# Optimization experiments

Measured on AMD Instinct MI355X. Metric: run time of the kernel, lower is better.

Reference implementation:

```python
import jax, jax.numpy as jnp
import numpy as np

N_NODES = 50000
N_EDGES = 300000
D_IN = 256
D_HID = 256
N_LAYERS = 3
D_OUT = 32
NUM_GRAPHS = 512


def setup_inputs() -> dict:
    key = jax.random.key(0)
    ks = jax.random.split(key, 10)
    x = jax.random.normal(ks[0], (N_NODES, D_IN), dtype=jnp.float32)
    edge_index = jax.random.randint(ks[1], (2, N_EDGES), 0, N_NODES, dtype=jnp.int64)
    batch = jnp.sort(jax.random.randint(ks[2], (N_NODES,), 0, NUM_GRAPHS, dtype=jnp.int64))
    # GraphConv params: out_i = relu(lin_rel(sum_j x_j) + lin_root(x_i)), bias in lin_rel.
    # in_channels == hidden_channels so all nc layers stack into one tensor.
    s = 1.0 / np.sqrt(D_HID)
    W_rel = jax.random.normal(ks[3], (N_LAYERS, D_HID, D_HID), dtype=jnp.float32) * s
    W_root = jax.random.normal(ks[4], (N_LAYERS, D_HID, D_HID), dtype=jnp.float32) * s
    b_conv = jax.random.normal(ks[5], (N_LAYERS, D_HID), dtype=jnp.float32) * s
    W1 = jax.random.normal(ks[6], (D_HID, 4 * D_HID), dtype=jnp.float32) * s
    b1 = jnp.zeros((4 * D_HID,), dtype=jnp.float32)
    W2 = jax.random.normal(ks[7], (4 * D_HID, D_OUT), dtype=jnp.float32) * (1.0 / np.sqrt(4 * D_HID))
    b2 = jnp.zeros((D_OUT,), dtype=jnp.float32)
    return {"x": x, "edge_index": edge_index, "batch": batch,
            "W_rel": W_rel, "W_root": W_root, "b_conv": b_conv,
            "W1": W1, "b1": b1, "W2": W2, "b2": b2,
            "num_graphs": NUM_GRAPHS}


def reference(x, edge_index, batch, W_rel, W_root, b_conv, W1, b1, W2, b2, num_graphs):
    src, dst = edge_index[0], edge_index[1]
    n = x.shape[0]
    # stacked GraphConv(aggr='add') layers with ReLU
    for i in range(W_rel.shape[0]):
        aggr = jax.ops.segment_sum(x[src], dst, num_segments=n)  # [N, d] gather+scatter-add
        x = jax.nn.relu(aggr @ W_rel[i] + x @ W_root[i] + b_conv[i])
    # global_add_pool over graph ids
    pooled = jax.ops.segment_sum(x, batch, num_segments=num_graphs)  # [G, d]
    h = jax.nn.relu(pooled @ W1 + b1)
    return jax.nn.sigmoid(h @ W2 + b2)
```

## Files before the change

### kernel.cpp

```cpp
#include <hip/hip_runtime.h>
#include <math.h>

#define NNODES 50000
#define MPAD   50048
#define D      256
#define K2     512
#define NEDGES 300000
#define NGRAPH 512
#define NLAYERS 3

#define SCB    256
#define NSCB   ((NNODES + SCB - 1) / SCB)

typedef __bf16 bf16x8 __attribute__((ext_vector_type(8)));
typedef float  f32x4  __attribute__((ext_vector_type(4)));

__device__ __forceinline__ ushort f2bf(float f) {
    unsigned u = __float_as_uint(f);
    unsigned r = (u + 0x7FFFu + ((u >> 16) & 1u)) >> 16;
    return (ushort)r;
}
__device__ __forceinline__ float bf2f(ushort b) {
    return __uint_as_float(((unsigned)b) << 16);
}

__device__ __forceinline__ void stage16(const ushort* g, ushort* l) {
    __builtin_amdgcn_global_load_lds(
        (const __attribute__((address_space(1))) unsigned*)g,
        (__attribute__((address_space(3))) unsigned*)l, 16, 0, 0);
}

__global__ __launch_bounds__(256)
void hist_kernel(const int* __restrict__ dst, int* __restrict__ deg, int nE) {
    int e = blockIdx.x * 256 + threadIdx.x;
    if (e < nE) atomicAdd(&deg[dst[e]], 1);
}

__global__ __launch_bounds__(SCB)
void scan_part_kernel(const int* __restrict__ deg, int* __restrict__ bsum) {
    __shared__ int red[SCB];
    int t = threadIdx.x;
    int i = blockIdx.x * SCB + t;
    red[t] = (i < NNODES) ? deg[i] : 0;
    __syncthreads();
#pragma unroll
    for (int off = SCB / 2; off > 0; off >>= 1) {
        if (t < off) red[t] += red[t + off];
        __syncthreads();
    }
    if (t == 0) bsum[blockIdx.x] = red[0];
}

__global__ __launch_bounds__(256)
void scan_bsum_kernel(const int* __restrict__ bsum, int* __restrict__ boff) {
    __shared__ int p[256];
    int t = threadIdx.x;
    p[t] = (t < NSCB) ? bsum[t] : 0;
    __syncthreads();
    for (int off = 1; off < 256; off <<= 1) {
        int v = (t >= off) ? p[t - off] : 0;
        __syncthreads();
        p[t] += v;
        __syncthreads();
    }
    if (t < NSCB) boff[t] = (t == 0) ? 0 : p[t - 1];
}

__global__ __launch_bounds__(SCB)
void scan_final_kernel(const int* __restrict__ deg, const int* __restrict__ boff,
                       int* __restrict__ row_start, int* __restrict__ cursor) {
    __shared__ int p[SCB];
    int t = threadIdx.x;
    int i = blockIdx.x * SCB + t;
    int v = (i < NNODES) ? deg[i] : 0;
    p[t] = v;
    __syncthreads();
    for (int off = 1; off < SCB; off <<= 1) {
        int u = (t >= off) ? p[t - off] : 0;
        __syncthreads();
        p[t] += u;
        __syncthreads();
    }
    int excl = boff[blockIdx.x] + p[t] - v;
    if (i < NNODES) {
        row_start[i] = excl;
        cursor[i] = excl;
    }
    if (blockIdx.x == 0 && t == 0) row_start[NNODES] = NEDGES;
}

__global__ __launch_bounds__(256)
void fill_kernel(const int* __restrict__ src, const int* __restrict__ dst,
                 int* __restrict__ cursor, int* __restrict__ e_src, int nE) {
    int e = blockIdx.x * 256 + threadIdx.x;
    if (e < nE) {
        int pos = atomicAdd(&cursor[dst[e]], 1);
        e_src[pos] = src[e];
    }
}

__global__ __launch_bounds__(256)
void gstart_kernel(const int* __restrict__ batch, int* __restrict__ gstart) {
    int g = blockIdx.x * 256 + threadIdx.x;
    if (g > NGRAPH) return;
    if (g == NGRAPH) { gstart[g] = NNODES; return; }
    int lo = 0, hi = NNODES;
    while (lo < hi) { int mid = (lo + hi) >> 1; if (batch[mid] < g) lo = mid + 1; else hi = mid; }
    gstart[g] = lo;
}

__global__ __launch_bounds__(256)
void prep_w_kernel(const float* __restrict__ W_rel, const float* __restrict__ W_root,
                   ushort* __restrict__ Wh, ushort* __restrict__ Wl) {
    int i = blockIdx.x * 256 + threadIdx.x;
    if (i >= NLAYERS * D * K2) return;
    int L = i / (D * K2);
    int rem = i % (D * K2);
    int n = rem / K2;
    int k = rem % K2;
    float v = (k < D) ? W_rel[(size_t)L * D * D + (size_t)k * D + n]
                      : W_root[(size_t)L * D * D + (size_t)(k - D) * D + n];
    ushort hi = f2bf(v);
    float  lo = v - bf2f(hi);
    Wh[i] = hi;
    Wl[i] = f2bf(lo);
}

__global__ __launch_bounds__(256)
void gather_f32_kernel(const float* __restrict__ x,
                       const int* __restrict__ row_start,
                       const int* __restrict__ e_src,
                       float* __restrict__ aggr) {
    int t = threadIdx.x;
    int n = blockIdx.x * 4 + (t >> 6);
    if (n >= NNODES) return;
    int lane = t & 63;
    int beg = row_start[n], end = row_start[n + 1];
    float a0 = 0.f, a1 = 0.f, a2 = 0.f, a3 = 0.f;
    int j = beg;
    for (; j + 4 <= end; j += 4) {
        int s0 = e_src[j], s1 = e_src[j + 1], s2 = e_src[j + 2], s3 = e_src[j + 3];
        float4 v0 = *reinterpret_cast<const float4*>(x + (size_t)s0 * D + lane * 4);
        float4 v1 = *reinterpret_cast<const float4*>(x + (size_t)s1 * D + lane * 4);
        float4 v2 = *reinterpret_cast<const float4*>(x + (size_t)s2 * D + lane * 4);
        float4 v3 = *reinterpret_cast<const float4*>(x + (size_t)s3 * D + lane * 4);
        a0 += v0.x + v1.x + v2.x + v3.x;
        a1 += v0.y + v1.y + v2.y + v3.y;
        a2 += v0.z + v1.z + v2.z + v3.z;
        a3 += v0.w + v1.w + v2.w + v3.w;
    }
    for (; j < end; ++j) {
        int s = e_src[j];
        float4 v = *reinterpret_cast<const float4*>(x + (size_t)s * D + lane * 4);
        a0 += v.x; a1 += v.y; a2 += v.z; a3 += v.w;
    }
    float4 o; o.x = a0; o.y = a1; o.z = a2; o.w = a3;
    *reinterpret_cast<float4*>(aggr + (size_t)n * D + lane * 4) = o;
}

#define GBM 128
#define GBN 128
#define GBK 32

__global__ __launch_bounds__(256)
void gemm_split_kernel(const float* __restrict__ A,
                       const float* __restrict__ X,
                       const ushort* __restrict__ Wh,
                       const ushort* __restrict__ Wl,
                       const float* __restrict__ bias,
                       float* __restrict__ out) {
    __shared__ ushort Ah[GBM * GBK];
    __shared__ ushort Al[GBM * GBK];
    __shared__ ushort Bh[GBN * GBK];
    __shared__ ushort Bl[GBN * GBK];

    int t = threadIdx.x;
    int wid = t >> 6, lane = t & 63;
    int m0 = blockIdx.x * GBM;
    int n0 = blockIdx.y * GBN;
    int wr = wid >> 1, wc = wid & 1;

    f32x4 acc[4][4];
#pragma unroll
    for (int m = 0; m < 4; ++m)
#pragma unroll
        for (int n = 0; n < 4; ++n)
            acc[m][n] = (f32x4){0.f, 0.f, 0.f, 0.f};

    int arow = t >> 1;
    int acb  = (t & 1) * 2;
    int aswz = (arow >> 1) & 3;
    int gr   = m0 + arow;
    bool arow_ok = (gr < NNODES);

    for (int k0 = 0; k0 < K2; k0 += GBK) {
        const float* Asrc = (k0 < D) ? A : X;
        int kk = k0 & (D - 1);

#pragma unroll
        for (int op = 0; op < 2; ++op) {
            int idx = op * 256 + wid * 64 + lane;
            int row = idx >> 2, sub = idx & 3;
            int kh = ((row >> 1) & 3) ^ sub;
            stage16(Wh + (size_t)(n0 + row) * K2 + k0 + kh * 8, Bh + (size_t)(op * 256 + wid * 64) * 8);
            stage16(Wl + (size_t)(n0 + row) * K2 + k0 + kh * 8, Bl + (size_t)(op * 256 + wid * 64) * 8);
        }

        {
            const float* base = Asrc + (size_t)gr * D + kk + acb * 8;
            float4 v0, v1, v2, v3;
            if (arow_ok) {
                v0 = *reinterpret_cast<const float4*>(base + 0);
                v1 = *reinterpret_cast<const float4*>(base + 4);
                v2 = *reinterpret_cast<const float4*>(base + 8);
                v3 = *reinterpret_cast<const float4*>(base + 12);
            } else {
                v0 = v1 = v2 = v3 = make_float4(0.f, 0.f, 0.f, 0.f);
            }
            float vv[16] = {v0.x, v0.y, v0.z, v0.w, v1.x, v1.y, v1.z, v1.w,
                            v2.x, v2.y, v2.z, v2.w, v3.x, v3.y, v3.z, v3.w};
            ushort hi[16], lo[16];
#pragma unroll
            for (int i = 0; i < 16; ++i) {
                hi[i] = f2bf(vv[i]);
                lo[i] = f2bf(vv[i] - bf2f(hi[i]));
            }
            int p0 = aswz ^ acb;
            int p1 = aswz ^ (acb + 1);
            *reinterpret_cast<uint4*>(&Ah[arow * GBK + p0 * 8]) = *reinterpret_cast<const uint4*>(&hi[0]);
            *reinterpret_cast<uint4*>(&Ah[arow * GBK + p1 * 8]) = *reinterpret_cast<const uint4*>(&hi[8]);
            *reinterpret_cast<uint4*>(&Al[arow * GBK + p0 * 8]) = *reinterpret_cast<const uint4*>(&lo[0]);
            *reinterpret_cast<uint4*>(&Al[arow * GBK + p1 * 8]) = *reinterpret_cast<const uint4*>(&lo[8]);
        }
        __syncthreads();

        bf16x8 ah[4], al[4], bh[4], bl[4];
        int half = lane >> 4;
#pragma unroll
        for (int m = 0; m < 4; ++m) {
            int row = wr * 64 + m * 16 + (lane & 15);
            int off = row * GBK + ((((row >> 1) & 3) ^ half) * 8);
            ah[m] = *reinterpret_cast<const bf16x8*>(&Ah[off]);
            al[m] = *reinterpret_cast<const bf16x8*>(&Al[off]);
        }
#pragma unroll
        for (int n = 0; n < 4; ++n) {
            int row = wc * 64 + n * 16 + (lane & 15);
            int off = row * GBK + ((((row >> 1) & 3) ^ half) * 8);
            bh[n] = *reinterpret_cast<const bf16x8*>(&Bh[off]);
            bl[n] = *reinterpret_cast<const bf16x8*>(&Bl[off]);
        }
#pragma unroll
        for (int m = 0; m < 4; ++m)
#pragma unroll
            for (int n = 0; n < 4; ++n) {
                acc[m][n] = __builtin_amdgcn_mfma_f32_16x16x32_bf16(ah[m], bh[n], acc[m][n], 0, 0, 0);
                acc[m][n] = __builtin_amdgcn_mfma_f32_16x16x32_bf16(ah[m], bl[n], acc[m][n], 0, 0, 0);
                acc[m][n] = __builtin_amdgcn_mfma_f32_16x16x32_bf16(al[m], bh[n], acc[m][n], 0, 0, 0);
            }
        __syncthreads();
    }

    int half = lane >> 4;
#pragma unroll
    for (int n = 0; n < 4; ++n) {
        int col = n0 + wc * 64 + n * 16 + (lane & 15);
        float bv = bias[col];
#pragma unroll
        for (int m = 0; m < 4; ++m) {
            int rbase = m0 + wr * 64 + m * 16 + half * 4;
#pragma unroll
            for (int j = 0; j < 4; ++j) {
                int r = rbase + j;
                if (r < NNODES)
                    out[(size_t)r * D + col] = fmaxf(acc[m][n][j] + bv, 0.f);
            }
        }
    }
}

__global__ __launch_bounds__(256)
void pool_seg_kernel(const float* __restrict__ x, const int* __restrict__ gstart,
                     float* __restrict__ pooled) {
    __shared__ float red[4][D];
    int g = blockIdx.x;
    int t = threadIdx.x, wid = t >> 6, lane = t & 63;
    int beg = gstart[g], end = gstart[g + 1];
    float a0 = 0.f, a1 = 0.f, a2 = 0.f, a3 = 0.f;
    for (int r = beg + wid; r < end; r += 4) {
        float4 v = *reinterpret_cast<const float4*>(x + (size_t)r * D + lane * 4);
        a0 += v.x; a1 += v.y; a2 += v.z; a3 += v.w;
    }
    red[wid][lane * 4 + 0] = a0;
    red[wid][lane * 4 + 1] = a1;
    red[wid][lane * 4 + 2] = a2;
    red[wid][lane * 4 + 3] = a3;
    __syncthreads();
    float s = red[0][t] + red[1][t] + red[2][t] + red[3][t];
    pooled[(size_t)g * D + t] = s;
}

__global__ __launch_bounds__(256)
void mlp1_kernel(const float* __restrict__ pooled, const float* __restrict__ W1,
                 const float* __restrict__ b1, float* __restrict__ h) {
    __shared__ float p[D];
    int g = blockIdx.x, t = threadIdx.x;
    p[t] = pooled[(size_t)g * D + t];
    __syncthreads();
    float4 acc = make_float4(0.f, 0.f, 0.f, 0.f);
    for (int k = 0; k < D; ++k) {
        float4 w = *reinterpret_cast<const float4*>(W1 + (size_t)k * 1024 + t * 4);
        float pv = p[k];
        acc.x += pv * w.x; acc.y += pv * w.y; acc.z += pv * w.z; acc.w += pv * w.w;
    }
    float4 b = *reinterpret_cast<const float4*>(b1 + t * 4);
    acc.x = fmaxf(acc.x + b.x, 0.f);
    acc.y = fmaxf(acc.y + b.y, 0.f);
    acc.z = fmaxf(acc.z + b.z, 0.f);
    acc.w = fmaxf(acc.w + b.w, 0.f);
    *reinterpret_cast<float4*>(h + (size_t)g * 1024 + t * 4) = acc;
}

__global__ __launch_bounds__(256)
void mlp2_kernel(const float* __restrict__ h, const float* __restrict__ W2,
                 const float* __restrict__ b2, float* __restrict__ out) {
    __shared__ float red[8][32];
    int g = blockIdx.x, t = threadIdx.x;
    int c = t & 31, kc = t >> 5;
    float s = 0.f;
    const float* hr = h + (size_t)g * 1024;
    for (int k = kc * 128; k < kc * 128 + 128; ++k)
        s += hr[k] * W2[(size_t)k * 32 + c];
    red[kc][c] = s;
    __syncthreads();
    if (t < 32) {
        float v = b2[t];
#pragma unroll
        for (int i = 0; i < 8; ++i) v += red[i][t];
        out[(size_t)g * 32 + t] = 1.f / (1.f + expf(-v));
    }
}

extern "C" void kernel_launch(void* const* d_in, const int* in_sizes, int n_in,
                              void* d_out, int out_size, void* d_ws, size_t ws_size,
                              hipStream_t stream) {
    const float* x      = (const float*)d_in[0];
    const int*   ei     = (const int*)d_in[1];
    const int*   batch  = (const int*)d_in[2];
    const float* W_rel  = (const float*)d_in[3];
    const float* W_root = (const float*)d_in[4];
    const float* b_conv = (const float*)d_in[5];
    const float* W1     = (const float*)d_in[6];
    const float* b1     = (const float*)d_in[7];
    const float* W2     = (const float*)d_in[8];
    const float* b2     = (const float*)d_in[9];
    float* outp = (float*)d_out;

    const size_t NF = (size_t)MPAD * D;
    float* aggr   = (float*)d_ws;
    float* buf0   = aggr + NF;
    float* buf1   = buf0 + NF;
    ushort* Wh    = (ushort*)(buf1 + NF);
    ushort* Wl    = Wh + (size_t)NLAYERS * D * K2;
    float* pooled = (float*)(Wl + (size_t)NLAYERS * D * K2);
    float* hbuf   = pooled + (size_t)NGRAPH * D;
    int* deg       = (int*)(hbuf + (size_t)NGRAPH * 1024);
    int* row_start = deg + NNODES;
    int* cursor    = row_start + NNODES + 1;
    int* e_src     = cursor + NNODES;
    int* gstart    = e_src + NEDGES;
    int* bsum      = gstart + NGRAPH + 1;
    int* boff      = bsum + NSCB;

    const int* srcp = ei;
    const int* dstp = ei + NEDGES;

    hipMemsetAsync(deg, 0, NNODES * sizeof(int), stream);
    hist_kernel<<<(NEDGES + 255) / 256, 256, 0, stream>>>(dstp, deg, NEDGES);
    scan_part_kernel<<<NSCB, SCB, 0, stream>>>(deg, bsum);
    scan_bsum_kernel<<<1, 256, 0, stream>>>(bsum, boff);
    scan_final_kernel<<<NSCB, SCB, 0, stream>>>(deg, boff, row_start, cursor);
    fill_kernel<<<(NEDGES + 255) / 256, 256, 0, stream>>>(srcp, dstp, cursor, e_src, NEDGES);
    gstart_kernel<<<3, 256, 0, stream>>>(batch, gstart);

    prep_w_kernel<<<(NLAYERS * D * K2 + 255) / 256, 256, 0, stream>>>(W_rel, W_root, Wh, Wl);

    int gatherBlocks = (NNODES + 3) / 4;
    dim3 ggrid(MPAD / GBM, D / GBN);

    const float* cur = x;
    float* nxt = buf0;
    for (int L = 0; L < NLAYERS; ++L) {
        gather_f32_kernel<<<gatherBlocks, 256, 0, stream>>>(cur, row_start, e_src, aggr);
        gemm_split_kernel<<<ggrid, 256, 0, stream>>>(aggr, cur,
                                                     Wh + (size_t)L * D * K2,
                                                     Wl + (size_t)L * D * K2,
                                                     b_conv + (size_t)L * D,
                                                     nxt);
        cur = nxt;
        nxt = (nxt == buf0) ? buf1 : buf0;
    }

    pool_seg_kernel<<<NGRAPH, 256, 0, stream>>>(cur, gstart, pooled);
    mlp1_kernel<<<NGRAPH, 256, 0, stream>>>(pooled, W1, b1, hbuf);
    mlp2_kernel<<<NGRAPH, 256, 0, stream>>>(hbuf, W2, b2, outp);
}
```

Baseline: 459.8 us.

## Store activations as pre-split bf16 hi/lo pairs across gather, GEMM and pool

Activations and aggregates are now kept as two bf16 arrays (high and residual) instead of fp32. The GEMM stages its A operand with async 16-byte copies into LDS rather than loading fp32 and splitting per tile, and the gather and pool kernels read and write the split format. This moves the split work out of the GEMM inner loop and lets A staging use the same path as B. In exchange it adds a one-time conversion kernel for x and extra conversion work in the gather and GEMM epilogue, and the GEMM epilogue now does scalar 2-byte stores. Gather traffic per edge stays about the same because two 8-byte loads replace one 16-byte load.

```diff
diff --git a/kernel.cpp b/kernel.cpp
--- a/kernel.cpp
+++ b/kernel.cpp
@@ -127,10 +127,32 @@
 }
 
 __global__ __launch_bounds__(256)
-void gather_f32_kernel(const float* __restrict__ x,
-                       const int* __restrict__ row_start,
-                       const int* __restrict__ e_src,
-                       float* __restrict__ aggr) {
+void cvt_x_kernel(const float* __restrict__ x, ushort* __restrict__ xh,
+                  ushort* __restrict__ xl) {
+    size_t base = ((size_t)blockIdx.x * 256 + threadIdx.x) * 8;
+    if (base >= (size_t)MPAD * D) return;
+    ushort h[8], l[8];
+    if (base < (size_t)NNODES * D) {
+        float4 v0 = *reinterpret_cast<const float4*>(x + base);
+        float4 v1 = *reinterpret_cast<const float4*>(x + base + 4);
+        float vv[8] = {v0.x, v0.y, v0.z, v0.w, v1.x, v1.y, v1.z, v1.w};
+#pragma unroll
+        for (int j = 0; j < 8; ++j) {
+            h[j] = f2bf(vv[j]);
+            l[j] = f2bf(vv[j] - bf2f(h[j]));
+        }
+    } else {
+#pragma unroll
+        for (int j = 0; j < 8; ++j) { h[j] = 0; l[j] = 0; }
+    }
+    *reinterpret_cast<uint4*>(xh + base) = *reinterpret_cast<uint4*>(h);
+    *reinterpret_cast<uint4*>(xl + base) = *reinterpret_cast<uint4*>(l);
+}
+
+__global__ __launch_bounds__(256)
+void gather_hl_kernel(const ushort* __restrict__ ph, const ushort* __restrict__ pl,
+                      const int* __restrict__ row_start, const int* __restrict__ e_src,
+                      ushort* __restrict__ gh, ushort* __restrict__ gl) {
     int t = threadIdx.x;
     int n = blockIdx.x * 4 + (t >> 6);
     if (n >= NNODES) return;
@@ -140,22 +162,39 @@
     int j = beg;
     for (; j + 4 <= end; j += 4) {
         int s0 = e_src[j], s1 = e_src[j + 1], s2 = e_src[j + 2], s3 = e_src[j + 3];
-        float4 v0 = *reinterpret_cast<const float4*>(x + (size_t)s0 * D + lane * 4);
-        float4 v1 = *reinterpret_cast<const float4*>(x + (size_t)s1 * D + lane * 4);
-        float4 v2 = *reinterpret_cast<const float4*>(x + (size_t)s2 * D + lane * 4);
-        float4 v3 = *reinterpret_cast<const float4*>(x + (size_t)s3 * D + lane * 4);
-        a0 += v0.x + v1.x + v2.x + v3.x;
-        a1 += v0.y + v1.y + v2.y + v3.y;
-        a2 += v0.z + v1.z + v2.z + v3.z;
-        a3 += v0.w + v1.w + v2.w + v3.w;
+        ushort4 h0 = *reinterpret_cast<const ushort4*>(ph + (size_t)s0 * D + lane * 4);
+        ushort4 l0 = *reinterpret_cast<const ushort4*>(pl + (size_t)s0 * D + lane * 4);
+        ushort4 h1 = *reinterpret_cast<const ushort4*>(ph + (size_t)s1 * D + lane * 4);
+        ushort4 l1 = *reinterpret_cast<const ushort4*>(pl + (size_t)s1 * D + lane * 4);
+        ushort4 h2 = *reinterpret_cast<const ushort4*>(ph + (size_t)s2 * D + lane * 4);
+        ushort4 l2 = *reinterpret_cast<const ushort4*>(pl + (size_t)s2 * D + lane * 4);
+        ushort4 h3 = *reinterpret_cast<const ushort4*>(ph + (size_t)s3 * D + lane * 4);
+        ushort4 l3 = *reinterpret_cast<const ushort4*>(pl + (size_t)s3 * D + lane * 4);
+        a0 += (bf2f(h0.x) + bf2f(l0.x)) + (bf2f(h1.x) + bf2f(l1.x)) +
+              (bf2f(h2.x) + bf2f(l2.x)) + (bf2f(h3.x) + bf2f(l3.x));
+        a1 += (bf2f(h0.y) + bf2f(l0.y)) + (bf2f(h1.y) + bf2f(l1.y)) +
+              (bf2f(h2.y) + bf2f(l2.y)) + (bf2f(h3.y) + bf2f(l3.y));
+        a2 += (bf2f(h0.z) + bf2f(l0.z)) + (bf2f(h1.z) + bf2f(l1.z)) +
+              (bf2f(h2.z) + bf2f(l2.z)) + (bf2f(h3.z) + bf2f(l3.z));
+        a3 += (bf2f(h0.w) + bf2f(l0.w)) + (bf2f(h1.w) + bf2f(l1.w)) +
+              (bf2f(h2.w) + bf2f(l2.w)) + (bf2f(h3.w) + bf2f(l3.w));
     }
     for (; j < end; ++j) {
         int s = e_src[j];
-        float4 v = *reinterpret_cast<const float4*>(x + (size_t)s * D + lane * 4);
-        a0 += v.x; a1 += v.y; a2 += v.z; a3 += v.w;
-    }
-    float4 o; o.x = a0; o.y = a1; o.z = a2; o.w = a3;
-    *reinterpret_cast<float4*>(aggr + (size_t)n * D + lane * 4) = o;
+        ushort4 h = *reinterpret_cast<const ushort4*>(ph + (size_t)s * D + lane * 4);
+        ushort4 l = *reinterpret_cast<const ushort4*>(pl + (size_t)s * D + lane * 4);
+        a0 += bf2f(h.x) + bf2f(l.x);
+        a1 += bf2f(h.y) + bf2f(l.y);
+        a2 += bf2f(h.z) + bf2f(l.z);
+        a3 += bf2f(h.w) + bf2f(l.w);
+    }
+    ushort4 oh, ol;
+    oh.x = f2bf(a0); ol.x = f2bf(a0 - bf2f(oh.x));
+    oh.y = f2bf(a1); ol.y = f2bf(a1 - bf2f(oh.y));
+    oh.z = f2bf(a2); ol.z = f2bf(a2 - bf2f(oh.z));
+    oh.w = f2bf(a3); ol.w = f2bf(a3 - bf2f(oh.w));
+    *reinterpret_cast<ushort4*>(gh + (size_t)n * D + lane * 4) = oh;
+    *reinterpret_cast<ushort4*>(gl + (size_t)n * D + lane * 4) = ol;
 }
 
 #define GBM 128
@@ -163,16 +202,15 @@
 #define GBK 32
 
 __global__ __launch_bounds__(256)
-void gemm_split_kernel(const float* __restrict__ A,
-                       const float* __restrict__ X,
-                       const ushort* __restrict__ Wh,
-                       const ushort* __restrict__ Wl,
-                       const float* __restrict__ bias,
-                       float* __restrict__ out) {
-    __shared__ ushort Ah[GBM * GBK];
-    __shared__ ushort Al[GBM * GBK];
-    __shared__ ushort Bh[GBN * GBK];
-    __shared__ ushort Bl[GBN * GBK];
+void gemm_hl_kernel(const ushort* __restrict__ Gh, const ushort* __restrict__ Gl,
+                    const ushort* __restrict__ Xh, const ushort* __restrict__ Xl,
+                    const ushort* __restrict__ Wh, const ushort* __restrict__ Wl,
+                    const float* __restrict__ bias,
+                    ushort* __restrict__ outh, ushort* __restrict__ outl) {
+    __shared__ ushort AhS[GBM * GBK];
+    __shared__ ushort AlS[GBM * GBK];
+    __shared__ ushort BhS[GBN * GBK];
+    __shared__ ushort BlS[GBN * GBK];
 
     int t = threadIdx.x;
     int wid = t >> 6, lane = t & 63;
@@ -187,14 +225,9 @@
         for (int n = 0; n < 4; ++n)
             acc[m][n] = (f32x4){0.f, 0.f, 0.f, 0.f};
 
-    int arow = t >> 1;
-    int acb  = (t & 1) * 2;
-    int aswz = (arow >> 1) & 3;
-    int gr   = m0 + arow;
-    bool arow_ok = (gr < NNODES);
-
     for (int k0 = 0; k0 < K2; k0 += GBK) {
-        const float* Asrc = (k0 < D) ? A : X;
+        const ushort* ah = (k0 < D) ? Gh : Xh;
+        const ushort* al = (k0 < D) ? Gl : Xl;
         int kk = k0 & (D - 1);
 
 #pragma unroll
@@ -202,61 +235,37 @@
             int idx = op * 256 + wid * 64 + lane;
             int row = idx >> 2, sub = idx & 3;
             int kh = ((row >> 1) & 3) ^ sub;
-            stage16(Wh + (size_t)(n0 + row) * K2 + k0 + kh * 8, Bh + (size_t)(op * 256 + wid * 64) * 8);
-            stage16(Wl + (size_t)(n0 + row) * K2 + k0 + kh * 8, Bl + (size_t)(op * 256 + wid * 64) * 8);
+            size_t ldso = (size_t)(op * 256 + wid * 64) * 8;
+            stage16(ah + (size_t)(m0 + row) * D + kk + kh * 8, AhS + ldso);
+            stage16(al + (size_t)(m0 + row) * D + kk + kh * 8, AlS + ldso);
+            stage16(Wh + (size_t)(n0 + row) * K2 + k0 + kh * 8, BhS + ldso);
+            stage16(Wl + (size_t)(n0 + row) * K2 + k0 + kh * 8, BlS + ldso);
         }
-
-        {
-            const float* base = Asrc + (size_t)gr * D + kk + acb * 8;
-            float4 v0, v1, v2, v3;
-            if (arow_ok) {
-                v0 = *reinterpret_cast<const float4*>(base + 0);
-                v1 = *reinterpret_cast<const float4*>(base + 4);
-                v2 = *reinterpret_cast<const float4*>(base + 8);
-                v3 = *reinterpret_cast<const float4*>(base + 12);
-            } else {
-                v0 = v1 = v2 = v3 = make_float4(0.f, 0.f, 0.f, 0.f);
-            }
-            float vv[16] = {v0.x, v0.y, v0.z, v0.w, v1.x, v1.y, v1.z, v1.w,
-                            v2.x, v2.y, v2.z, v2.w, v3.x, v3.y, v3.z, v3.w};
-            ushort hi[16], lo[16];
-#pragma unroll
-            for (int i = 0; i < 16; ++i) {
-                hi[i] = f2bf(vv[i]);
-                lo[i] = f2bf(vv[i] - bf2f(hi[i]));
-            }
-            int p0 = aswz ^ acb;
-            int p1 = aswz ^ (acb + 1);
-            *reinterpret_cast<uint4*>(&Ah[arow * GBK + p0 * 8]) = *reinterpret_cast<const uint4*>(&hi[0]);
-            *reinterpret_cast<uint4*>(&Ah[arow * GBK + p1 * 8]) = *reinterpret_cast<const uint4*>(&hi[8]);
-            *reinterpret_cast<uint4*>(&Al[arow * GBK + p0 * 8]) = *reinterpret_cast<const uint4*>(&lo[0]);
-            *reinterpret_cast<uint4*>(&Al[arow * GBK + p1 * 8]) = *reinterpret_cast<const uint4*>(&lo[8]);
-        }
-        __syncthreads();
-
-        bf16x8 ah[4], al[4], bh[4], bl[4];
+        __syncthreads();
+
+        bf16x8 fah[4], fal[4], fbh[4], fbl[4];
         int half = lane >> 4;
 #pragma unroll
         for (int m = 0; m < 4; ++m) {
             int row = wr * 64 + m * 16 + (lane & 15);
             int off = row * GBK + ((((row >> 1) & 3) ^ half) * 8);
-            ah[m] = *reinterpret_cast<const bf16x8*>(&Ah[off]);
-            al[m] = *reinterpret_cast<const bf16x8*>(&Al[off]);
+            fah[m] = *reinterpret_cast<const bf16x8*>(&AhS[off]);
+            fal[m] = *reinterpret_cast<const bf16x8*>(&AlS[off]);
         }
 #pragma unroll
         for (int n = 0; n < 4; ++n) {
             int row = wc * 64 + n * 16 + (lane & 15);
             int off = row * GBK + ((((row >> 1) & 3) ^ half) * 8);
-            bh[n] = *reinterpret_cast<const bf16x8*>(&Bh[off]);
-            bl[n] = *reinterpret_cast<const bf16x8*>(&Bl[off]);
+            fbh[n] = *reinterpret_cast<const bf16x8*>(&BhS[off]);
+            fbl[n] = *reinterpret_cast<const bf16x8*>(&BlS[off]);
         }
 #pragma unroll
         for (int m = 0; m < 4; ++m)
 #pragma unroll
             for (int n = 0; n < 4; ++n) {
-                acc[m][n] = __builtin_amdgcn_mfma_f32_16x16x32_bf16(ah[m], bh[n], acc[m][n], 0, 0, 0);
-                acc[m][n] = __builtin_amdgcn_mfma_f32_16x16x32_bf16(ah[m], bl[n], acc[m][n], 0, 0, 0);
-                acc[m][n] = __builtin_amdgcn_mfma_f32_16x16x32_bf16(al[m], bh[n], acc[m][n], 0, 0, 0);
+                acc[m][n] = __builtin_amdgcn_mfma_f32_16x16x32_bf16(fah[m], fbh[n], acc[m][n], 0, 0, 0);
+                acc[m][n] = __builtin_amdgcn_mfma_f32_16x16x32_bf16(fah[m], fbl[n], acc[m][n], 0, 0, 0);
+                acc[m][n] = __builtin_amdgcn_mfma_f32_16x16x32_bf16(fal[m], fbh[n], acc[m][n], 0, 0, 0);
             }
         __syncthreads();
     }
@@ -272,24 +281,32 @@
 #pragma unroll
             for (int j = 0; j < 4; ++j) {
                 int r = rbase + j;
-                if (r < NNODES)
-                    out[(size_t)r * D + col] = fmaxf(acc[m][n][j] + bv, 0.f);
+                if (r < NNODES) {
+                    float v = fmaxf(acc[m][n][j] + bv, 0.f);
+                    ushort hv = f2bf(v);
+                    outh[(size_t)r * D + col] = hv;
+                    outl[(size_t)r * D + col] = f2bf(v - bf2f(hv));
+                }
             }
         }
     }
 }
 
 __global__ __launch_bounds__(256)
-void pool_seg_kernel(const float* __restrict__ x, const int* __restrict__ gstart,
-                     float* __restrict__ pooled) {
+void pool_seg_kernel(const ushort* __restrict__ ph, const ushort* __restrict__ pl,
+                     const int* __restrict__ gstart, float* __restrict__ pooled) {
     __shared__ float red[4][D];
     int g = blockIdx.x;
     int t = threadIdx.x, wid = t >> 6, lane = t & 63;
     int beg = gstart[g], end = gstart[g + 1];
     float a0 = 0.f, a1 = 0.f, a2 = 0.f, a3 = 0.f;
     for (int r = beg + wid; r < end; r += 4) {
-        float4 v = *reinterpret_cast<const float4*>(x + (size_t)r * D + lane * 4);
-        a0 += v.x; a1 += v.y; a2 += v.z; a3 += v.w;
+        ushort4 h = *reinterpret_cast<const ushort4*>(ph + (size_t)r * D + lane * 4);
+        ushort4 l = *reinterpret_cast<const ushort4*>(pl + (size_t)r * D + lane * 4);
+        a0 += bf2f(h.x) + bf2f(l.x);
+        a1 += bf2f(h.y) + bf2f(l.y);
+        a2 += bf2f(h.z) + bf2f(l.z);
+        a3 += bf2f(h.w) + bf2f(l.w);
     }
     red[wid][lane * 4 + 0] = a0;
     red[wid][lane * 4 + 1] = a1;
@@ -357,11 +374,14 @@
     float* outp = (float*)d_out;
 
     const size_t NF = (size_t)MPAD * D;
-    float* aggr   = (float*)d_ws;
-    float* buf0   = aggr + NF;
-    float* buf1   = buf0 + NF;
-    ushort* Wh    = (ushort*)(buf1 + NF);
-    ushort* Wl    = Wh + (size_t)NLAYERS * D * K2;
+    ushort* xh = (ushort*)d_ws;
+    ushort* xl = xh + NF;
+    ushort* yh = xl + NF;
+    ushort* yl = yh + NF;
+    ushort* gh = yl + NF;
+    ushort* gl = gh + NF;
+    ushort* Wh = gl + NF;
+    ushort* Wl = Wh + (size_t)NLAYERS * D * K2;
     float* pooled = (float*)(Wl + (size_t)NLAYERS * D * K2);
     float* hbuf   = pooled + (size_t)NGRAPH * D;
     int* deg       = (int*)(hbuf + (size_t)NGRAPH * 1024);
@@ -384,24 +404,27 @@
     gstart_kernel<<<3, 256, 0, stream>>>(batch, gstart);
 
     prep_w_kernel<<<(NLAYERS * D * K2 + 255) / 256, 256, 0, stream>>>(W_rel, W_root, Wh, Wl);
+    cvt_x_kernel<<<(int)((NF / 8 + 255) / 256), 256, 0, stream>>>(x, xh, xl);
 
     int gatherBlocks = (NNODES + 3) / 4;
     dim3 ggrid(MPAD / GBM, D / GBN);
 
-    const float* cur = x;
-    float* nxt = buf0;
+    const ushort* curh = xh; const ushort* curl = xl;
+    ushort* nxth = yh;       ushort* nxtl = yl;
     for (int L = 0; L < NLAYERS; ++L) {
-        gather_f32_kernel<<<gatherBlocks, 256, 0, stream>>>(cur, row_start, e_src, aggr);
-        gemm_split_kernel<<<ggrid, 256, 0, stream>>>(aggr, cur,
-                                                     Wh + (size_t)L * D * K2,
-                                                     Wl + (size_t)L * D * K2,
-                                                     b_conv + (size_t)L * D,
-                                                     nxt);
-        cur = nxt;
-        nxt = (nxt == buf0) ? buf1 : buf0;
-    }
-
-    pool_seg_kernel<<<NGRAPH, 256, 0, stream>>>(cur, gstart, pooled);
+        gather_hl_kernel<<<gatherBlocks, 256, 0, stream>>>(curh, curl, row_start, e_src, gh, gl);
+        gemm_hl_kernel<<<ggrid, 256, 0, stream>>>(gh, gl, curh, curl,
+                                                  Wh + (size_t)L * D * K2,
+                                                  Wl + (size_t)L * D * K2,
+                                                  b_conv + (size_t)L * D,
+                                                  nxth, nxtl);
+        const ushort* th = curh; const ushort* tl = curl;
+        curh = nxth; curl = nxtl;
+        nxth = (ushort*)th; nxtl = (ushort*)tl;
+        if (L == 0) { nxth = xh; nxtl = xl; }
+    }
+
+    pool_seg_kernel<<<NGRAPH, 256, 0, stream>>>(curh, curl, gstart, pooled);
     mlp1_kernel<<<NGRAPH, 256, 0, stream>>>(pooled, W1, b1, hbuf);
     mlp2_kernel<<<NGRAPH, 256, 0, stream>>>(hbuf, W2, b2, outp);
 }
```

Result: slower. 475.9 us (+3.5%).
